# Performance work log

Hardware: AMD Instinct MI355X
Metric: run time of the kernel (lower is better)

## Reference

```python
import jax, jax.numpy as jnp
import numpy as np
from functools import partial


def lstm(x, Wx, Wh, b, act):
    """Keras LSTM. x:[B,T,F]. Gate order i,f,c,o. Returns (all_h:[B,T,H], last_h:[B,H])."""
    B, T, _ = x.shape
    H = Wh.shape[0]
    xz = jnp.einsum('btf,fg->btg', x, Wx) + b  # precompute input projections
    def step(carry, xz_t):
        h, c = carry
        z = xz_t + h @ Wh
        i, f, g, o = jnp.split(z, 4, axis=-1)
        i = jax.nn.sigmoid(i); f = jax.nn.sigmoid(f)
        g = act(g); o = jax.nn.sigmoid(o)
        c = f * c + i * g
        h = o * act(c)
        return (h, c), h
    init = (jnp.zeros((B, H), x.dtype), jnp.zeros((B, H), x.dtype))
    (h_last, _), hs = jax.lax.scan(step, init, jnp.swapaxes(xz, 0, 1))
    return jnp.swapaxes(hs, 0, 1), h_last


def gru(x, Wx, Wh, b):
    """Keras GRU with reset_after=True. b:[2,3H]. Gate order z,r,h. Returns last h."""
    B, T, _ = x.shape
    H = Wh.shape[0]
    xz = jnp.einsum('btf,fg->btg', x, Wx) + b[0]
    def step(h, xz_t):
        rec = h @ Wh + b[1]
        xz_z, xz_r, xz_h = jnp.split(xz_t, 3, axis=-1)
        r_z, r_r, r_h = jnp.split(rec, 3, axis=-1)
        z = jax.nn.sigmoid(xz_z + r_z)
        r = jax.nn.sigmoid(xz_r + r_r)
        hh = jnp.tanh(xz_h + r * r_h)
        h = z * h + (1.0 - z) * hh
        return h, None
    h0 = jnp.zeros((B, H), x.dtype)
    h_last, _ = jax.lax.scan(step, h0, jnp.swapaxes(xz, 0, 1))
    return h_last


def setup_inputs() -> dict:
    key = jax.random.key(0)
    ks = jax.random.split(key, 32)
    s = 0.05  # small init so relu-LSTM stays numerically stable over 64 steps
    d = {}
    d['keypoint_data'] = jax.random.normal(ks[0], (256, 64, 1662), jnp.float32)
    d['img_data'] = jax.random.normal(ks[1], (256, 64, 2048), jnp.float32)
    # keypoint LSTM stack: 1662->64->128->64, gates=4H
    d['kW1x'] = s * jax.random.normal(ks[2], (1662, 256), jnp.float32)
    d['kW1h'] = s * jax.random.normal(ks[3], (64, 256), jnp.float32)
    d['kb1'] = jnp.zeros((256,), jnp.float32)
    d['kW2x'] = s * jax.random.normal(ks[4], (64, 512), jnp.float32)
    d['kW2h'] = s * jax.random.normal(ks[5], (128, 512), jnp.float32)
    d['kb2'] = jnp.zeros((512,), jnp.float32)
    d['kW3x'] = s * jax.random.normal(ks[6], (128, 256), jnp.float32)
    d['kW3h'] = s * jax.random.normal(ks[7], (64, 256), jnp.float32)
    d['kb3'] = jnp.zeros((256,), jnp.float32)
    # keypoint dense heads
    d['kD1w'] = s * jax.random.normal(ks[8], (64, 64), jnp.float32)
    d['kD1b'] = jnp.zeros((64,), jnp.float32)
    d['kD2w'] = s * jax.random.normal(ks[9], (64, 32), jnp.float32)
    d['kD2b'] = jnp.zeros((32,), jnp.float32)
    # img branch: LSTM 2048->64 (tanh), GRU 64->8 (reset_after bias [2,24])
    d['iWx'] = s * jax.random.normal(ks[10], (2048, 256), jnp.float32)
    d['iWh'] = s * jax.random.normal(ks[11], (64, 256), jnp.float32)
    d['ib'] = jnp.zeros((256,), jnp.float32)
    d['gWx'] = s * jax.random.normal(ks[12], (64, 24), jnp.float32)
    d['gWh'] = s * jax.random.normal(ks[13], (8, 24), jnp.float32)
    d['gb'] = jnp.zeros((2, 24), jnp.float32)
    d['iDw'] = s * jax.random.normal(ks[14], (8, 8), jnp.float32)
    d['iDb'] = jnp.zeros((8,), jnp.float32)
    # final dense on concat([img(8), key(32)]) -> num_classes
    d['fW'] = s * jax.random.normal(ks[15], (40, 10), jnp.float32)
    d['fb'] = jnp.zeros((10,), jnp.float32)
    return d


def reference(keypoint_data, img_data,
              kW1x, kW1h, kb1, kW2x, kW2h, kb2, kW3x, kW3h, kb3,
              kD1w, kD1b, kD2w, kD2b,
              iWx, iWh, ib, gWx, gWh, gb, iDw, iDb, fW, fb):
    relu = jax.nn.relu
    # keypoint branch: 3 relu-LSTMs
    h, _ = lstm(keypoint_data, kW1x, kW1h, kb1, relu)
    h, _ = lstm(h, kW2x, kW2h, kb2, relu)
    _, h = lstm(h, kW3x, kW3h, kb3, relu)  # return_sequences=False
    h = relu(h @ kD1w + kD1b)
    key_out = relu(h @ kD2w + kD2b)  # [B,32]
    # img branch: tanh LSTM -> GRU -> (dropout=identity at inference) -> dense
    hs, _ = lstm(img_data, iWx, iWh, ib, jnp.tanh)
    g = gru(hs, gWx, gWh, gb)  # [B,8]
    img_out = relu(g @ iDw + iDb)  # [B,8]
    combined = jnp.concatenate([img_out, key_out], axis=-1)  # [B,40]
    return jax.nn.softmax(combined @ fW + fb, axis=-1)
```

## Files before the change

kernel.cpp:

```cpp
#include <hip/hip_runtime.h>


typedef short bf16x8 __attribute__((ext_vector_type(8)));
typedef float f32x4 __attribute__((ext_vector_type(4)));

__device__ __forceinline__ unsigned f2bf(float x) {
    unsigned u = __float_as_uint(x);
    return (u + 0x7FFFu + ((u >> 16) & 1u)) >> 16;
}
__device__ __forceinline__ float bf2f(unsigned b) { return __uint_as_float(b << 16); }
__device__ __forceinline__ float sigmoidf_(float x) { return 1.f / (1.f + __expf(-x)); }
__device__ __forceinline__ float tanhf_(float x) {
    float e = __expf(2.f * x);
    return 1.f - 2.f / (e + 1.f);
}

__device__ __forceinline__ void cvt2(float x0, float x1, unsigned& hp, unsigned& lp) {
    unsigned h;
    asm("v_cvt_pk_bf16_f32 %0, %1, %2" : "=v"(h) : "v"(x0), "v"(x1));
    float a0 = __uint_as_float(h << 16);
    float a1 = __uint_as_float(h & 0xffff0000u);
    unsigned l;
    asm("v_cvt_pk_bf16_f32 %0, %1, %2" : "=v"(l) : "v"(x0 - a0), "v"(x1 - a1));
    hp = h; lp = l;
}

template<int K, int N>
__device__ __forceinline__ void split_w(const float* __restrict__ W,
                                        unsigned short* __restrict__ hi,
                                        unsigned short* __restrict__ lo, int item) {
    int kt = item / N;
    int n  = item % N;
    unsigned uh[16], ul[16];
#pragma unroll
    for (int p = 0; p < 16; p++) {
        unsigned h2[2], l2[2];
#pragma unroll
        for (int e = 0; e < 2; e++) {
            int k = kt * 32 + p * 2 + e;
            float x = (k < K) ? W[(size_t)k * N + n] : 0.f;
            unsigned hb = f2bf(x);
            h2[e] = hb;
            l2[e] = f2bf(x - bf2f(hb));
        }
        uh[p] = h2[0] | (h2[1] << 16);
        ul[p] = l2[0] | (l2[1] << 16);
    }
    size_t off = (size_t)(kt * N + n) * 32;
    uint4* dh = (uint4*)(hi + off);
    uint4* dl = (uint4*)(lo + off);
#pragma unroll
    for (int c = 0; c < 4; c++) {
        uint4 v; v.x = uh[c*4]; v.y = uh[c*4+1]; v.z = uh[c*4+2]; v.w = uh[c*4+3];
        dh[c] = v;
        uint4 u; u.x = ul[c*4]; u.y = ul[c*4+1]; u.z = ul[c*4+2]; u.w = ul[c*4+3];
        dl[c] = u;
    }
}

__global__ __launch_bounds__(256) void split_all(
    const float* kW1x, const float* iWx, const float* kW2x, const float* kW3x,
    unsigned short* w1h, unsigned short* w1l, unsigned short* wih, unsigned short* wil,
    unsigned short* w2h, unsigned short* w2l, unsigned short* w3h, unsigned short* w3l) {
    int wid = blockIdx.x * 256 + threadIdx.x;
    if (wid < 13312)       split_w<1662, 256>(kW1x, w1h, w1l, wid);
    else if (wid < 29696)  split_w<2048, 256>(iWx,  wih, wil, wid - 13312);
    else if (wid < 30720)  split_w<64,   512>(kW2x, w2h, w2l, wid - 29696);
    else if (wid < 31744)  split_w<128,  256>(kW3x, w3h, w3l, wid - 30720);
}

__global__ __launch_bounds__(256, 2) void gemm_rd(
    const float* __restrict__ A, const unsigned short* __restrict__ Bhi,
    const unsigned short* __restrict__ Blo, const float* __restrict__ bias,
    float* __restrict__ out0, float* __restrict__ out1,
    int Kreal, int Kt, int Nfull) {
    const int m0  = blockIdx.x * 128;
    const int n0  = blockIdx.y * 128;
    const int ks  = blockIdx.z;
    const int nks = gridDim.z;
    const int ktChunk = Kt / nks;
    const int kt0 = ks * ktChunk;
    const int G   = (ktChunk + 1) / 2;
    const int tid = threadIdx.x;
    const int lane = tid & 63;
    const int wv   = tid >> 6;
    const int l15  = lane & 15;
    const int q    = lane >> 4;
    const int row  = tid >> 1;
    const int kc   = tid & 1;

    __shared__ unsigned short Ah[2][2][128 * 40], Al[2][2][128 * 40];

    f32x4 acc[8][2];
#pragma unroll
    for (int i = 0; i < 8; i++)
#pragma unroll
        for (int j = 0; j < 2; j++) acc[i][j] = (f32x4){0.f, 0.f, 0.f, 0.f};

    auto loadA = [&](int g, float* r) {
        int kb = (kt0 + 2 * g + kc) * 32;
        const float* ap = A + (size_t)(m0 + row) * Kreal + kb;
        if (kb + 32 <= Kreal) {
#pragma unroll
            for (int j = 0; j < 16; j++) {
                float2 p = *(const float2*)(ap + 2 * j);
                r[2*j] = p.x; r[2*j+1] = p.y;
            }
        } else {
#pragma unroll
            for (int j = 0; j < 16; j++) {
                int gk = kb + 2 * j;
                r[2*j]   = (gk     < Kreal) ? ap[2*j]   : 0.f;
                r[2*j+1] = (gk + 1 < Kreal) ? ap[2*j+1] : 0.f;
            }
        }
    };
    auto writeA = [&](int buf, const float* r) {
        unsigned ph[16], pl[16];
#pragma unroll
        for (int p = 0; p < 16; p++) cvt2(r[2*p], r[2*p+1], ph[p], pl[p]);
        uint4* dh = (uint4*)&Ah[buf][kc][row * 40];
        uint4* dl = (uint4*)&Al[buf][kc][row * 40];
#pragma unroll
        for (int c = 0; c < 4; c++) {
            uint4 v; v.x = ph[c*4]; v.y = ph[c*4+1]; v.z = ph[c*4+2]; v.w = ph[c*4+3];
            dh[c] = v;
            uint4 u; u.x = pl[c*4]; u.y = pl[c*4+1]; u.z = pl[c*4+2]; u.w = pl[c*4+3];
            dl[c] = u;
        }
    };
    auto loadB = [&](int g, bf16x8* bh, bf16x8* bl) {
#pragma unroll
        for (int sub = 0; sub < 2; sub++)
#pragma unroll
            for (int nt = 0; nt < 2; nt++) {
                size_t boff = ((size_t)(kt0 + 2 * g + sub) * Nfull + n0 + wv * 32 + nt * 16 + l15) * 32 + q * 8;
                bh[sub * 2 + nt] = *(const bf16x8*)(Bhi + boff);
                bl[sub * 2 + nt] = *(const bf16x8*)(Blo + boff);
            }
    };
    auto compute = [&](int buf, const bf16x8* bh, const bf16x8* bl) {
#pragma unroll
        for (int sub = 0; sub < 2; sub++)
#pragma unroll
            for (int mt = 0; mt < 8; mt++) {
                int o = (mt * 16 + l15) * 40 + q * 8;
                bf16x8 ah = *(const bf16x8*)&Ah[buf][sub][o];
                bf16x8 al = *(const bf16x8*)&Al[buf][sub][o];
#pragma unroll
                for (int nt = 0; nt < 2; nt++) {
                    acc[mt][nt] = __builtin_amdgcn_mfma_f32_16x16x32_bf16(ah, bh[sub*2+nt], acc[mt][nt], 0, 0, 0);
                    acc[mt][nt] = __builtin_amdgcn_mfma_f32_16x16x32_bf16(ah, bl[sub*2+nt], acc[mt][nt], 0, 0, 0);
                    acc[mt][nt] = __builtin_amdgcn_mfma_f32_16x16x32_bf16(al, bh[sub*2+nt], acc[mt][nt], 0, 0, 0);
                }
            }
    };

    float  rA[32], rB[32];
    bf16x8 bhA[4], blA[4], bhB[4], blB[4];
    loadA(0, rA);
    writeA(0, rA);
    loadB(0, bhA, blA);
    if (G > 1) loadA(1, rB);
    __syncthreads();

    for (int g = 0; g < G; g += 2) {
        if (g + 1 < G) loadB(g + 1, bhB, blB);
        if (g + 2 < G) loadA(g + 2, rA);
        compute(0, bhA, blA);
        if (g + 1 < G) writeA(1, rB);
        __syncthreads();
        if (g + 1 < G) {
            if (g + 2 < G) loadB(g + 2, bhA, blA);
            if (g + 3 < G) loadA(g + 3, rB);
            compute(1, bhB, blB);
            if (g + 2 < G) writeA(0, rA);
            __syncthreads();
        }
    }

    float* op = (ks == 0) ? out0 : out1;
#pragma unroll
    for (int nt = 0; nt < 2; nt++) {
        int gcol = n0 + wv * 32 + nt * 16 + l15;
        float bv = (ks == 0) ? bias[gcol] : 0.f;
#pragma unroll
        for (int mt = 0; mt < 8; mt++)
#pragma unroll
            for (int r = 0; r < 4; r++) {
                int grow = m0 + mt * 16 + q * 4 + r;
                op[(size_t)grow * Nfull + gcol] = acc[mt][nt][r] + bv;
            }
    }
}

__global__ __launch_bounds__(256) void lstm_h64(
    int nA,
    const float* __restrict__ xA0, const float* __restrict__ xA1,
    const float* __restrict__ WhA, float* __restrict__ hA, int actA,
    const float* __restrict__ xB0, const float* __restrict__ xB1,
    const float* __restrict__ WhB, float* __restrict__ hB, int actB) {
    int bid = blockIdx.x;
    bool sec = bid >= nA;
    int b = sec ? bid - nA : bid;
    const float* x0 = sec ? xB0 : xA0;
    const float* x1 = sec ? xB1 : xA1;
    const float* Wh = sec ? WhB : WhA;
    float* hout     = sec ? hB  : hA;
    int act         = sec ? actB : actA;
    bool has1 = (x1 != nullptr);

    int g = threadIdx.x;
    float w[64];
#pragma unroll
    for (int k = 0; k < 64; k++) w[k] = Wh[k * 256 + g];

    __shared__ alignas(16) float hs[64];
    __shared__ float za[256];
    if (g < 64) hs[g] = 0.f;
    float c = 0.f;
    __syncthreads();

    const float* x0r = x0 + (size_t)b * 64 * 256;
    const float* x1r = has1 ? x1 + (size_t)b * 64 * 256 : x0r;
    float* hr = hout + (size_t)b * 64 * 64;
    bool isc = (g >= 128) && (g < 192);
    float cur = x0r[g] + (has1 ? x1r[g] : 0.f);
    for (int t = 0; t < 64; t++) {
        float nxt = 0.f;
        if (t < 63) {
            nxt = x0r[(t + 1) * 256 + g];
            if (has1) nxt += x1r[(t + 1) * 256 + g];
        }
        float z0 = cur, z1 = 0.f, z2 = 0.f, z3 = 0.f;
#pragma unroll
        for (int kk = 0; kk < 16; kk++) {
            float4 h4 = *(const float4*)&hs[kk * 4];
            z0 = fmaf(h4.x, w[kk * 4 + 0], z0);
            z1 = fmaf(h4.y, w[kk * 4 + 1], z1);
            z2 = fmaf(h4.z, w[kk * 4 + 2], z2);
            z3 = fmaf(h4.w, w[kk * 4 + 3], z3);
        }
        float z = (z0 + z1) + (z2 + z3);
        float a;
        if (isc) a = (act == 0) ? fmaxf(z, 0.f) : tanhf_(z);
        else     a = sigmoidf_(z);
        za[g] = a;
        __syncthreads();
        if (g < 64) {
            float iv = za[g], fv = za[64 + g], cd = za[128 + g], ov = za[192 + g];
            c = fmaf(fv, c, iv * cd);
            float ca = (act == 0) ? fmaxf(c, 0.f) : tanhf_(c);
            float h = ov * ca;
            hs[g] = h;
            hr[t * 64 + g] = h;
        }
        __syncthreads();
        cur = nxt;
    }
}

__global__ __launch_bounds__(512, 2) void lstm_h128(
    const float* __restrict__ xz, const float* __restrict__ Wh, float* __restrict__ hout) {
    int b = blockIdx.x;
    int g = threadIdx.x;
    float w[128];
#pragma unroll
    for (int k = 0; k < 128; k++) w[k] = Wh[k * 512 + g];

    __shared__ alignas(16) float hs[128];
    __shared__ float za[512];
    if (g < 128) hs[g] = 0.f;
    float c = 0.f;
    __syncthreads();

    const float* xzr = xz + (size_t)b * 64 * 512;
    float* hr = hout + (size_t)b * 64 * 128;
    bool isc = (g >= 256) && (g < 384);
    float cur = xzr[g];
    for (int t = 0; t < 64; t++) {
        float nxt = 0.f;
        if (t < 63) nxt = xzr[(t + 1) * 512 + g];
        float z0 = cur, z1 = 0.f, z2 = 0.f, z3 = 0.f;
#pragma unroll
        for (int kk = 0; kk < 32; kk++) {
            float4 h4 = *(const float4*)&hs[kk * 4];
            z0 = fmaf(h4.x, w[kk * 4 + 0], z0);
            z1 = fmaf(h4.y, w[kk * 4 + 1], z1);
            z2 = fmaf(h4.z, w[kk * 4 + 2], z2);
            z3 = fmaf(h4.w, w[kk * 4 + 3], z3);
        }
        float z = (z0 + z1) + (z2 + z3);
        float a = isc ? fmaxf(z, 0.f) : sigmoidf_(z);
        za[g] = a;
        __syncthreads();
        if (g < 128) {
            float iv = za[g], fv = za[128 + g], cd = za[256 + g], ov = za[384 + g];
            c = fmaf(fv, c, iv * cd);
            float h = ov * fmaxf(c, 0.f);
            hs[g] = h;
            hr[t * 128 + g] = h;
        }
        __syncthreads();
        cur = nxt;
    }
}

__global__ __launch_bounds__(64) void gru_kernel(
    const float* __restrict__ hsimg, const float* __restrict__ gWx,
    const float* __restrict__ gWh, const float* __restrict__ gb,
    float* __restrict__ glast) {
    int b = blockIdx.x;
    int qq = threadIdx.x;
    int col = (qq < 24) ? qq : 0;
    float wx[64], wh[8];
#pragma unroll
    for (int k = 0; k < 64; k++) wx[k] = gWx[k * 24 + col];
#pragma unroll
    for (int k = 0; k < 8; k++)  wh[k] = gWh[k * 24 + col];
    float b0 = gb[col], b1 = gb[24 + col];

    float hval = 0.f;
    const float* hb = hsimg + (size_t)b * 64 * 64;
    float cur = hb[qq];
    for (int t = 0; t < 64; t++) {
        float nxt = (t < 63) ? hb[(t + 1) * 64 + qq] : 0.f;
        float s0 = b0, s1 = 0.f, s2 = 0.f, s3 = 0.f;
#pragma unroll
        for (int k = 0; k < 64; k += 4) {
            s0 = fmaf(__shfl(cur, k + 0), wx[k + 0], s0);
            s1 = fmaf(__shfl(cur, k + 1), wx[k + 1], s1);
            s2 = fmaf(__shfl(cur, k + 2), wx[k + 2], s2);
            s3 = fmaf(__shfl(cur, k + 3), wx[k + 3], s3);
        }
        float sx = (s0 + s1) + (s2 + s3);
        float sr = b1;
#pragma unroll
        for (int k = 0; k < 8; k++) sr = fmaf(__shfl(hval, k), wh[k], sr);
        float xzz = __shfl(sx, qq),      rzz = __shfl(sr, qq);
        float xzr = __shfl(sx, 8 + qq),  rzr = __shfl(sr, 8 + qq);
        float xzh = __shfl(sx, 16 + qq), rzh = __shfl(sr, 16 + qq);
        float zz = sigmoidf_(xzz + rzz);
        float rv = sigmoidf_(xzr + rzr);
        float hc = tanhf_(xzh + rv * rzh);
        hval = zz * hval + (1.f - zz) * hc;
        cur = nxt;
    }
    if (qq < 8) glast[b * 8 + qq] = hval;
}

__global__ __launch_bounds__(64) void final_head(
    const float* __restrict__ h3seq, const float* __restrict__ glast,
    const float* __restrict__ kD1w, const float* __restrict__ kD1b,
    const float* __restrict__ kD2w, const float* __restrict__ kD2b,
    const float* __restrict__ iDw,  const float* __restrict__ iDb,
    const float* __restrict__ fW,   const float* __restrict__ fb,
    float* __restrict__ outp) {
    int b = blockIdx.x * 64 + threadIdx.x;
    float h3[64];
#pragma unroll
    for (int k = 0; k < 64; k++) h3[k] = h3seq[((size_t)b * 64 + 63) * 64 + k];
    float d1[64];
#pragma unroll
    for (int j = 0; j < 64; j++) {
        float s = kD1b[j];
#pragma unroll
        for (int k = 0; k < 64; k++) s = fmaf(h3[k], kD1w[k * 64 + j], s);
        d1[j] = fmaxf(s, 0.f);
    }
    float d2[32];
#pragma unroll
    for (int j = 0; j < 32; j++) {
        float s = kD2b[j];
#pragma unroll
        for (int k = 0; k < 64; k++) s = fmaf(d1[k], kD2w[k * 32 + j], s);
        d2[j] = fmaxf(s, 0.f);
    }
    float gi[8];
#pragma unroll
    for (int k = 0; k < 8; k++) gi[k] = glast[b * 8 + k];
    float io[8];
#pragma unroll
    for (int j = 0; j < 8; j++) {
        float s = iDb[j];
#pragma unroll
        for (int k = 0; k < 8; k++) s = fmaf(gi[k], iDw[k * 8 + j], s);
        io[j] = fmaxf(s, 0.f);
    }
    float lg[10];
#pragma unroll
    for (int j = 0; j < 10; j++) {
        float s = fb[j];
#pragma unroll
        for (int k = 0; k < 8; k++)  s = fmaf(io[k], fW[k * 10 + j], s);
#pragma unroll
        for (int k = 0; k < 32; k++) s = fmaf(d2[k], fW[(8 + k) * 10 + j], s);
        lg[j] = s;
    }
    float mx = lg[0];
#pragma unroll
    for (int j = 1; j < 10; j++) mx = fmaxf(mx, lg[j]);
    float den = 0.f, ex[10];
#pragma unroll
    for (int j = 0; j < 10; j++) { ex[j] = __expf(lg[j] - mx); den += ex[j]; }
    float inv = 1.f / den;
#pragma unroll
    for (int j = 0; j < 10; j++) outp[b * 10 + j] = ex[j] * inv;
}

extern "C" void kernel_launch(void* const* d_in, const int* in_sizes, int n_in,
                              void* d_out, int out_size, void* d_ws, size_t ws_size,
                              hipStream_t stream) {
    const float* keypoint = (const float*)d_in[0];
    const float* img      = (const float*)d_in[1];
    const float* kW1x = (const float*)d_in[2];
    const float* kW1h = (const float*)d_in[3];
    const float* kb1  = (const float*)d_in[4];
    const float* kW2x = (const float*)d_in[5];
    const float* kW2h = (const float*)d_in[6];
    const float* kb2  = (const float*)d_in[7];
    const float* kW3x = (const float*)d_in[8];
    const float* kW3h = (const float*)d_in[9];
    const float* kb3  = (const float*)d_in[10];
    const float* kD1w = (const float*)d_in[11];
    const float* kD1b = (const float*)d_in[12];
    const float* kD2w = (const float*)d_in[13];
    const float* kD2b = (const float*)d_in[14];
    const float* iWx  = (const float*)d_in[15];
    const float* iWh  = (const float*)d_in[16];
    const float* ib   = (const float*)d_in[17];
    const float* gWx  = (const float*)d_in[18];
    const float* gWh  = (const float*)d_in[19];
    const float* gb   = (const float*)d_in[20];
    const float* iDw  = (const float*)d_in[21];
    const float* iDb  = (const float*)d_in[22];
    const float* fW   = (const float*)d_in[23];
    const float* fb   = (const float*)d_in[24];
    float* outp = (float*)d_out;

    char* ws = (char*)d_ws;
    const size_t MB16 = (size_t)16384 * 256 * 4;
    float* r1a = (float*)(ws);
    float* r1b = (float*)(ws + MB16);
    float* r2a = (float*)(ws + 2 * MB16);
    float* r2b = (float*)(ws + 3 * MB16);
    size_t off = 4 * MB16;
    float* h1seq = (float*)(ws + off); off += (size_t)16384 * 64 * 4;
    float* h2seq = (float*)(ws + off); off += (size_t)16384 * 128 * 4;
    float* hsimg = (float*)(ws + off); off += (size_t)16384 * 64 * 4;
    float* glast = (float*)(ws + off); off += (size_t)256 * 8 * 4;
    unsigned short* w1h = (unsigned short*)(ws + off); off += (size_t)52 * 256 * 32 * 2;
    unsigned short* w1l = (unsigned short*)(ws + off); off += (size_t)52 * 256 * 32 * 2;
    unsigned short* wih = (unsigned short*)(ws + off); off += (size_t)64 * 256 * 32 * 2;
    unsigned short* wil = (unsigned short*)(ws + off); off += (size_t)64 * 256 * 32 * 2;
    unsigned short* w2h = (unsigned short*)(ws + off); off += (size_t)2 * 512 * 32 * 2;
    unsigned short* w2l = (unsigned short*)(ws + off); off += (size_t)2 * 512 * 32 * 2;
    unsigned short* w3h = (unsigned short*)(ws + off); off += (size_t)4 * 256 * 32 * 2;
    unsigned short* w3l = (unsigned short*)(ws + off); off += (size_t)4 * 256 * 32 * 2;
    float* xz2   = r2a;
    float* h3seq = h1seq;

    split_all<<<124, 256, 0, stream>>>(kW1x, iWx, kW2x, kW3x,
                                       w1h, w1l, wih, wil, w2h, w2l, w3h, w3l);
    gemm_rd<<<dim3(128, 2, 2), 256, 0, stream>>>(keypoint, w1h, w1l, kb1, r1a, r1b, 1662, 52, 256);
    gemm_rd<<<dim3(128, 2, 2), 256, 0, stream>>>(img, wih, wil, ib, r2a, r2b, 2048, 64, 256);
    lstm_h64<<<512, 256, 0, stream>>>(256, r1a, r1b, kW1h, h1seq, 0, r2a, r2b, iWh, hsimg, 1);
    gemm_rd<<<dim3(128, 4, 1), 256, 0, stream>>>(h1seq, w2h, w2l, kb2, xz2, xz2, 64, 2, 512);
    lstm_h128<<<256, 512, 0, stream>>>(xz2, kW2h, h2seq);
    gemm_rd<<<dim3(128, 2, 2), 256, 0, stream>>>(h2seq, w3h, w3l, kb3, r1a, r1b, 128, 4, 256);
    lstm_h64<<<256, 256, 0, stream>>>(256, r1a, r1b, kW3h, h3seq, 0, r1a, r1b, kW3h, h3seq, 0);
    gru_kernel<<<256, 64, 0, stream>>>(hsimg, gWx, gWh, gb, glast);
    final_head<<<4, 64, 0, stream>>>(h3seq, glast, kD1w, kD1b, kD2w, kD2b,
                                     iDw, iDb, fW, fb, outp);
    (void)in_sizes; (void)n_in; (void)out_size; (void)ws_size;
}
```

Measured before the change: 687.3 us.

## Remove per-step barrier in LSTM recurrences and fuse GRU into image LSTM

Result: faster. 667.1 us (-2.9%).

```diff
diff --git a/kernel.cpp b/kernel.cpp
--- a/kernel.cpp
+++ b/kernel.cpp
@@ -199,7 +199,9 @@
     const float* __restrict__ xA0, const float* __restrict__ xA1,
     const float* __restrict__ WhA, float* __restrict__ hA, int actA,
     const float* __restrict__ xB0, const float* __restrict__ xB1,
-    const float* __restrict__ WhB, float* __restrict__ hB, int actB) {
+    const float* __restrict__ WhB, float* __restrict__ hB, int actB,
+    const float* __restrict__ gWx, const float* __restrict__ gWh,
+    const float* __restrict__ gb,  float* __restrict__ glast) {
     int bid = blockIdx.x;
     bool sec = bid >= nA;
     int b = sec ? bid - nA : bid;
@@ -208,22 +210,25 @@
     const float* Wh = sec ? WhB : WhA;
     float* hout     = sec ? hB  : hA;
     int act         = sec ? actB : actA;
-    bool has1 = (x1 != nullptr);
+    bool has1  = (x1 != nullptr);
+    bool fused = sec && (glast != nullptr);
 
     int g = threadIdx.x;
-    float w[64];
-#pragma unroll
-    for (int k = 0; k < 64; k++) w[k] = Wh[k * 256 + g];
-
-    __shared__ alignas(16) float hs[64];
-    __shared__ float za[256];
-    if (g < 64) hs[g] = 0.f;
+    int w = g >> 6;
+    int l = g & 63;
+    float wreg[64];
+#pragma unroll
+    for (int k = 0; k < 64; k++) wreg[k] = Wh[k * 256 + g];
+
+    __shared__ alignas(16) float hs4[4][64];
+    __shared__ float za[2][256];
+    __shared__ alignas(16) float hseq[64][64];
+    hs4[w][l] = 0.f;
     float c = 0.f;
-    __syncthreads();
 
     const float* x0r = x0 + (size_t)b * 64 * 256;
     const float* x1r = has1 ? x1 + (size_t)b * 64 * 256 : x0r;
-    float* hr = hout + (size_t)b * 64 * 64;
+    float* hr = hout ? hout + (size_t)b * 64 * 64 : nullptr;
     bool isc = (g >= 128) && (g < 192);
     float cur = x0r[g] + (has1 ? x1r[g] : 0.f);
     for (int t = 0; t < 64; t++) {
@@ -235,28 +240,64 @@
         float z0 = cur, z1 = 0.f, z2 = 0.f, z3 = 0.f;
 #pragma unroll
         for (int kk = 0; kk < 16; kk++) {
-            float4 h4 = *(const float4*)&hs[kk * 4];
-            z0 = fmaf(h4.x, w[kk * 4 + 0], z0);
-            z1 = fmaf(h4.y, w[kk * 4 + 1], z1);
-            z2 = fmaf(h4.z, w[kk * 4 + 2], z2);
-            z3 = fmaf(h4.w, w[kk * 4 + 3], z3);
+            float4 h4 = *(const float4*)&hs4[w][kk * 4];
+            z0 = fmaf(h4.x, wreg[kk * 4 + 0], z0);
+            z1 = fmaf(h4.y, wreg[kk * 4 + 1], z1);
+            z2 = fmaf(h4.z, wreg[kk * 4 + 2], z2);
+            z3 = fmaf(h4.w, wreg[kk * 4 + 3], z3);
         }
         float z = (z0 + z1) + (z2 + z3);
         float a;
         if (isc) a = (act == 0) ? fmaxf(z, 0.f) : tanhf_(z);
         else     a = sigmoidf_(z);
-        za[g] = a;
+        int p = t & 1;
+        za[p][g] = a;
         __syncthreads();
-        if (g < 64) {
-            float iv = za[g], fv = za[64 + g], cd = za[128 + g], ov = za[192 + g];
-            c = fmaf(fv, c, iv * cd);
-            float ca = (act == 0) ? fmaxf(c, 0.f) : tanhf_(c);
-            float h = ov * ca;
-            hs[g] = h;
-            hr[t * 64 + g] = h;
-        }
-        __syncthreads();
+        float iv = za[p][l], fv = za[p][64 + l], cd = za[p][128 + l], ov = za[p][192 + l];
+        c = fmaf(fv, c, iv * cd);
+        float ca = (act == 0) ? fmaxf(c, 0.f) : tanhf_(c);
+        float h = ov * ca;
+        hs4[w][l] = h;
+        if (w == 0) {
+            if (hr) hr[t * 64 + l] = h;
+            if (fused) hseq[t][l] = h;
+        }
         cur = nxt;
+    }
+
+    if (fused && w == 0) {
+        int qq = l;
+        int col = (qq < 24) ? qq : 0;
+        float wx[64], wh[8];
+#pragma unroll
+        for (int k = 0; k < 64; k++) wx[k] = gWx[k * 24 + col];
+#pragma unroll
+        for (int k = 0; k < 8; k++)  wh[k] = gWh[k * 24 + col];
+        float b0 = gb[col], b1 = gb[24 + col];
+        float hval = 0.f;
+        for (int t = 0; t < 64; t++) {
+            float s0 = b0, s1 = 0.f, s2 = 0.f, s3 = 0.f;
+#pragma unroll
+            for (int kk = 0; kk < 16; kk++) {
+                float4 h4 = *(const float4*)&hseq[t][kk * 4];
+                s0 = fmaf(h4.x, wx[kk * 4 + 0], s0);
+                s1 = fmaf(h4.y, wx[kk * 4 + 1], s1);
+                s2 = fmaf(h4.z, wx[kk * 4 + 2], s2);
+                s3 = fmaf(h4.w, wx[kk * 4 + 3], s3);
+            }
+            float sx = (s0 + s1) + (s2 + s3);
+            float sr = b1;
+#pragma unroll
+            for (int k = 0; k < 8; k++) sr = fmaf(__shfl(hval, k), wh[k], sr);
+            float xzz = __shfl(sx, qq),      rzz = __shfl(sr, qq);
+            float xzr = __shfl(sx, 8 + qq),  rzr = __shfl(sr, 8 + qq);
+            float xzh = __shfl(sx, 16 + qq), rzh = __shfl(sr, 16 + qq);
+            float zz = sigmoidf_(xzz + rzz);
+            float rv = sigmoidf_(xzr + rzr);
+            float hc = tanhf_(xzh + rv * rzh);
+            hval = zz * hval + (1.f - zz) * hc;
+        }
+        if (qq < 8) glast[b * 8 + qq] = hval;
     }
 }
 
@@ -264,15 +305,17 @@
     const float* __restrict__ xz, const float* __restrict__ Wh, float* __restrict__ hout) {
     int b = blockIdx.x;
     int g = threadIdx.x;
-    float w[128];
-#pragma unroll
-    for (int k = 0; k < 128; k++) w[k] = Wh[k * 512 + g];
-
-    __shared__ alignas(16) float hs[128];
-    __shared__ float za[512];
-    if (g < 128) hs[g] = 0.f;
-    float c = 0.f;
-    __syncthreads();
+    int w = g >> 6;
+    int l = g & 63;
+    float wreg[128];
+#pragma unroll
+    for (int k = 0; k < 128; k++) wreg[k] = Wh[k * 512 + g];
+
+    __shared__ alignas(16) float hs8[8][128];
+    __shared__ float za[2][512];
+    hs8[w][l] = 0.f;
+    hs8[w][64 + l] = 0.f;
+    float c0 = 0.f, c1 = 0.f;
 
     const float* xzr = xz + (size_t)b * 64 * 512;
     float* hr = hout + (size_t)b * 64 * 128;
@@ -284,69 +327,35 @@
         float z0 = cur, z1 = 0.f, z2 = 0.f, z3 = 0.f;
 #pragma unroll
         for (int kk = 0; kk < 32; kk++) {
-            float4 h4 = *(const float4*)&hs[kk * 4];
-            z0 = fmaf(h4.x, w[kk * 4 + 0], z0);
-            z1 = fmaf(h4.y, w[kk * 4 + 1], z1);
-            z2 = fmaf(h4.z, w[kk * 4 + 2], z2);
-            z3 = fmaf(h4.w, w[kk * 4 + 3], z3);
+            float4 h4 = *(const float4*)&hs8[w][kk * 4];
+            z0 = fmaf(h4.x, wreg[kk * 4 + 0], z0);
+            z1 = fmaf(h4.y, wreg[kk * 4 + 1], z1);
+            z2 = fmaf(h4.z, wreg[kk * 4 + 2], z2);
+            z3 = fmaf(h4.w, wreg[kk * 4 + 3], z3);
         }
         float z = (z0 + z1) + (z2 + z3);
         float a = isc ? fmaxf(z, 0.f) : sigmoidf_(z);
-        za[g] = a;
+        int p = t & 1;
+        za[p][g] = a;
         __syncthreads();
-        if (g < 128) {
-            float iv = za[g], fv = za[128 + g], cd = za[256 + g], ov = za[384 + g];
-            c = fmaf(fv, c, iv * cd);
-            float h = ov * fmaxf(c, 0.f);
-            hs[g] = h;
-            hr[t * 128 + g] = h;
-        }
-        __syncthreads();
+        {
+            float iv = za[p][l],      fv = za[p][128 + l];
+            float cd = za[p][256 + l], ov = za[p][384 + l];
+            c0 = fmaf(fv, c0, iv * cd);
+            float h = ov * fmaxf(c0, 0.f);
+            hs8[w][l] = h;
+            if (w == 0) hr[t * 128 + l] = h;
+        }
+        {
+            float iv = za[p][64 + l],  fv = za[p][192 + l];
+            float cd = za[p][320 + l], ov = za[p][448 + l];
+            c1 = fmaf(fv, c1, iv * cd);
+            float h = ov * fmaxf(c1, 0.f);
+            hs8[w][64 + l] = h;
+            if (w == 0) hr[t * 128 + 64 + l] = h;
+        }
         cur = nxt;
     }
-}
-
-__global__ __launch_bounds__(64) void gru_kernel(
-    const float* __restrict__ hsimg, const float* __restrict__ gWx,
-    const float* __restrict__ gWh, const float* __restrict__ gb,
-    float* __restrict__ glast) {
-    int b = blockIdx.x;
-    int qq = threadIdx.x;
-    int col = (qq < 24) ? qq : 0;
-    float wx[64], wh[8];
-#pragma unroll
-    for (int k = 0; k < 64; k++) wx[k] = gWx[k * 24 + col];
-#pragma unroll
-    for (int k = 0; k < 8; k++)  wh[k] = gWh[k * 24 + col];
-    float b0 = gb[col], b1 = gb[24 + col];
-
-    float hval = 0.f;
-    const float* hb = hsimg + (size_t)b * 64 * 64;
-    float cur = hb[qq];
-    for (int t = 0; t < 64; t++) {
-        float nxt = (t < 63) ? hb[(t + 1) * 64 + qq] : 0.f;
-        float s0 = b0, s1 = 0.f, s2 = 0.f, s3 = 0.f;
-#pragma unroll
-        for (int k = 0; k < 64; k += 4) {
-            s0 = fmaf(__shfl(cur, k + 0), wx[k + 0], s0);
-            s1 = fmaf(__shfl(cur, k + 1), wx[k + 1], s1);
-            s2 = fmaf(__shfl(cur, k + 2), wx[k + 2], s2);
-            s3 = fmaf(__shfl(cur, k + 3), wx[k + 3], s3);
-        }
-        float sx = (s0 + s1) + (s2 + s3);
-        float sr = b1;
-#pragma unroll
-        for (int k = 0; k < 8; k++) sr = fmaf(__shfl(hval, k), wh[k], sr);
-        float xzz = __shfl(sx, qq),      rzz = __shfl(sr, qq);
-        float xzr = __shfl(sx, 8 + qq),  rzr = __shfl(sr, 8 + qq);
-        float xzh = __shfl(sx, 16 + qq), rzh = __shfl(sr, 16 + qq);
-        float zz = sigmoidf_(xzz + rzz);
-        float rv = sigmoidf_(xzr + rzr);
-        float hc = tanhf_(xzh + rv * rzh);
-        hval = zz * hval + (1.f - zz) * hc;
-        cur = nxt;
-    }
-    if (qq < 8) glast[b * 8 + qq] = hval;
 }
 
 __global__ __launch_bounds__(64) void final_head(
@@ -447,7 +456,6 @@
     size_t off = 4 * MB16;
     float* h1seq = (float*)(ws + off); off += (size_t)16384 * 64 * 4;
     float* h2seq = (float*)(ws + off); off += (size_t)16384 * 128 * 4;
-    float* hsimg = (float*)(ws + off); off += (size_t)16384 * 64 * 4;
     float* glast = (float*)(ws + off); off += (size_t)256 * 8 * 4;
     unsigned short* w1h = (unsigned short*)(ws + off); off += (size_t)52 * 256 * 32 * 2;
     unsigned short* w1l = (unsigned short*)(ws + off); off += (size_t)52 * 256 * 32 * 2;
@@ -464,12 +472,15 @@
                                        w1h, w1l, wih, wil, w2h, w2l, w3h, w3l);
     gemm_rd<<<dim3(128, 2, 2), 256, 0, stream>>>(keypoint, w1h, w1l, kb1, r1a, r1b, 1662, 52, 256);
     gemm_rd<<<dim3(128, 2, 2), 256, 0, stream>>>(img, wih, wil, ib, r2a, r2b, 2048, 64, 256);
-    lstm_h64<<<512, 256, 0, stream>>>(256, r1a, r1b, kW1h, h1seq, 0, r2a, r2b, iWh, hsimg, 1);
+    lstm_h64<<<512, 256, 0, stream>>>(256, r1a, r1b, kW1h, h1seq, 0,
+                                           r2a, r2b, iWh, nullptr, 1,
+                                           gWx, gWh, gb, glast);
     gemm_rd<<<dim3(128, 4, 1), 256, 0, stream>>>(h1seq, w2h, w2l, kb2, xz2, xz2, 64, 2, 512);
     lstm_h128<<<256, 512, 0, stream>>>(xz2, kW2h, h2seq);
     gemm_rd<<<dim3(128, 2, 2), 256, 0, stream>>>(h2seq, w3h, w3l, kb3, r1a, r1b, 128, 4, 256);
-    lstm_h64<<<256, 256, 0, stream>>>(256, r1a, r1b, kW3h, h3seq, 0, r1a, r1b, kW3h, h3seq, 0);
-    gru_kernel<<<256, 64, 0, stream>>>(hsimg, gWx, gWh, gb, glast);
+    lstm_h64<<<256, 256, 0, stream>>>(256, r1a, r1b, kW3h, h3seq, 0,
+                                           nullptr, nullptr, nullptr, nullptr, 0,
+                                           nullptr, nullptr, nullptr, nullptr);
     final_head<<<4, 64, 0, stream>>>(h3seq, glast, kD1w, kD1b, kD2w, kD2b,
                                      iDw, iDb, fW, fb, outp);
     (void)in_sizes; (void)n_in; (void)out_size; (void)ws_size;
```
